# Performance work log

Measured on AMD Instinct MI355X. Metric: run time of the kernel, lower is better.

The kernel has to match this reference:

```python
import jax, jax.numpy as jnp
import numpy as np

NUM_HEADS = 16
CAPACITY = 512
ROPE_BASE = 10000.0

def _rope_factor(positions, dim):
    # freqs = exp(linspace(0,-1,dim//2) * log(base)), shape (dim//2,)
    freqs = jnp.exp(jnp.linspace(0.0, -1.0, dim // 2) * jnp.log(jnp.float32(ROPE_BASE)))
    angles = positions[..., None] * freqs            # (..., seq, dim//2)
    return jnp.concatenate([jnp.sin(angles), jnp.cos(angles)], axis=-1)  # (..., seq, dim)

def setup_inputs() -> dict:
    key = jax.random.key(0)
    ks = jax.random.split(key, 6)
    B, Sq, Skv, D = 4, 4096, 4096, 1024
    return {
        "query_seq": jax.random.normal(ks[0], (B, Sq, D), jnp.float32),
        "value_seq": jax.random.normal(ks[1], (B, Skv, D), jnp.float32),
        "router_w": jax.random.normal(ks[2], (1, D), jnp.float32) * 0.02,
        "q_w": jax.random.normal(ks[3], (D, D), jnp.float32) * 0.02,
        "kv_w": jax.random.normal(ks[4], (2 * D, D), jnp.float32) * 0.02,
        "out_w": jax.random.normal(ks[5], (D, D), jnp.float32) * 0.02,
    }

def reference(query_seq, value_seq, router_w, q_w, kv_w, out_w):
    B, Sq, D = query_seq.shape
    Skv = value_seq.shape[1]
    H, C = NUM_HEADS, CAPACITY
    d = D // H

    # router + top-k capacity selection over the sequence dim
    rw = jnp.einsum("bsd,od->bs", query_seq, router_w).astype(jnp.float32)  # (B,Sq)
    top_w, top_idx = jax.lax.top_k(rw, C)                                   # (B,C)

    # gather selected queries
    resampled = jnp.take_along_axis(query_seq, top_idx[:, :, None], axis=1)  # (B,C,D)

    q = jnp.einsum("bcd,ed->bce", resampled, q_w)        # (B,C,H*d)
    kv = jnp.einsum("bsd,ed->bse", value_seq, kv_w)      # (B,Skv,2*H*d)
    k, v = jnp.split(kv, 2, axis=-1)

    q = q.reshape(B, C, H, d).transpose(0, 2, 1, 3)      # (B,H,C,d)
    k = k.reshape(B, Skv, H, d).transpose(0, 2, 1, 3)    # (B,H,Skv,d)
    v = v.reshape(B, Skv, H, d).transpose(0, 2, 1, 3)

    # RoPE-style elementwise modulation (faithful to source: x * cat(sin, cos))
    q_pos = top_idx.astype(jnp.float32)[:, None, :]      # (B,1,C)
    q = q * _rope_factor(q_pos, d)                       # (B,H,C,d)
    k_pos = jnp.arange(Skv, dtype=jnp.float32)[None, :]  # (1,Skv)
    k = k * _rope_factor(k_pos, d)[None]                 # broadcast over (B,H)

    # SDPA
    scores = jnp.einsum("bhcd,bhsd->bhcs", q, k) / jnp.sqrt(jnp.float32(d))
    att = jnp.einsum("bhcs,bhsd->bhcd", jax.nn.softmax(scores, axis=-1), v)

    att = att.transpose(0, 2, 1, 3).reshape(B, C, H * d)  # (B,C,D)
    att = jnp.einsum("bce,de->bcd", att, out_w)           # (B,C,D)

    # weighted scatter back to full sequence
    src = att * top_w[:, :, None]
    out = jnp.zeros_like(query_seq).at[jnp.arange(B)[:, None], top_idx].set(src)
    return out
```

## Files before the change

kernel.cpp:

```cpp
#include <hip/hip_runtime.h>
#include <hip/hip_bf16.h>

#define B_  4
#define SQ  4096
#define SKV 4096
#define DM  1024
#define NH  16
#define HD  64
#define CAP 512

#define ASPLIT 4
#define KVPER  (SKV / ASPLIT)
#define AITERS (KVPER / 64)

typedef __attribute__((ext_vector_type(8))) short    short8;
typedef __attribute__((ext_vector_type(8))) __bf16   bf16v8;
typedef __attribute__((ext_vector_type(4))) float    f32x4;
typedef __attribute__((ext_vector_type(4))) unsigned short ushort4v;

static __device__ __forceinline__ unsigned short f2bf(float f) {
    unsigned u = __float_as_uint(f);
    u += 0x7FFFu + ((u >> 16) & 1u);
    return (unsigned short)(u >> 16);
}

static __device__ __forceinline__ f32x4 mfma_bf16(short8 a, short8 b, f32x4 c) {
    return __builtin_amdgcn_mfma_f32_16x16x32_bf16(
        __builtin_bit_cast(bf16v8, a), __builtin_bit_cast(bf16v8, b), c, 0, 0, 0);
}

#define GLD16(gp, lp)                                                              \
    __builtin_amdgcn_global_load_lds(                                              \
        (__attribute__((address_space(1))) void*)(gp),                             \
        (__attribute__((address_space(3))) void*)(lp), 16, 0, 0)

__global__ void __launch_bounds__(256) k_convert(const float* __restrict__ in,
                                                 unsigned short* __restrict__ out) {
    size_t i = (size_t)blockIdx.x * 256 + threadIdx.x;
    float4 f = ((const float4*)in)[i];
    ushort4v o = { f2bf(f.x), f2bf(f.y), f2bf(f.z), f2bf(f.w) };
    ((ushort4v*)out)[i] = o;
}

__global__ void __launch_bounds__(256) k_rope(float* __restrict__ tab) {
    int g = blockIdx.x * 256 + threadIdx.x;
    int pos = g >> 6, i = g & 63, j = i & 31;
    float freq = expf(-(float)j * (logf(10000.0f) / 31.0f));
    float ang  = (float)pos * freq;
    tab[g] = (i < 32) ? sinf(ang) : cosf(ang);
}

__global__ void __launch_bounds__(256) k_router(const float* __restrict__ q,
                                                const float* __restrict__ wv,
                                                float* __restrict__ rw) {
    int row  = blockIdx.x * 4 + (threadIdx.x >> 6);
    int lane = threadIdx.x & 63;
    const float* p  = q  + (size_t)row * DM + lane * 16;
    const float* wp = wv + lane * 16;
    float s = 0.f;
#pragma unroll
    for (int j = 0; j < 4; j++) {
        float4 a = ((const float4*)p)[j];
        float4 b = ((const float4*)wp)[j];
        s += a.x * b.x + a.y * b.y + a.z * b.z + a.w * b.w;
    }
#pragma unroll
    for (int m = 32; m > 0; m >>= 1) s += __shfl_xor(s, m, 64);
    if (lane == 0) rw[row] = s;
}

__global__ void __launch_bounds__(1024) k_topk(const float* __restrict__ rw,
                                               int* __restrict__ sel,
                                               float* __restrict__ selw) {
    __shared__ unsigned long long keys[4096];
    int b = blockIdx.x, t = threadIdx.x;
    for (int i = t; i < 4096; i += 1024) {
        float v = rw[b * 4096 + i];
        unsigned u = __float_as_uint(v);
        u = (u & 0x80000000u) ? ~u : (u | 0x80000000u);
        keys[i] = ((unsigned long long)(~u) << 32) | (unsigned)i;
    }
    __syncthreads();
    for (int k = 2; k <= 4096; k <<= 1)
        for (int j = k >> 1; j > 0; j >>= 1) {
            for (int i = t; i < 4096; i += 1024) {
                int ixj = i ^ j;
                if (ixj > i) {
                    bool up = ((i & k) == 0);
                    unsigned long long a = keys[i], c = keys[ixj];
                    if ((a > c) == up) { keys[i] = c; keys[ixj] = a; }
                }
            }
            __syncthreads();
        }
    for (int i = t; i < 512; i += 1024) {
        unsigned idx = (unsigned)(keys[i] & 0xFFFFFFFFu);
        sel[b * 512 + i]  = (int)idx;
        selw[b * 512 + i] = rw[b * 4096 + idx];
    }
}

__global__ void __launch_bounds__(256) k_gather(const float* __restrict__ q,
                                                const int* __restrict__ sel,
                                                unsigned short* __restrict__ out) {
    int row = blockIdx.x;
    int b = row >> 9;
    int s = sel[row];
    const float4* src = (const float4*)(q + ((size_t)b * SQ + s) * DM);
    ushort4v* dst = (ushort4v*)(out + (size_t)row * DM);
    float4 f = src[threadIdx.x];
    ushort4v o = { f2bf(f.x), f2bf(f.y), f2bf(f.z), f2bf(f.w) };
    dst[threadIdx.x] = o;
}

template <int MODE>
__global__ void __launch_bounds__(256) k_gemm(
    const unsigned short* __restrict__ A,
    const unsigned short* __restrict__ Bw,
    int M, int N, int K,
    const float* __restrict__ rope_tab,
    const int* __restrict__ sel,
    const float* __restrict__ selw,
    unsigned short* __restrict__ ok,
    unsigned short* __restrict__ ov,
    unsigned short* __restrict__ obf,
    float* __restrict__ of) {
    __shared__ unsigned short lA[128 * 32];
    __shared__ unsigned short lB[128 * 32];
    const int tid = threadIdx.x;
    const int w = tid >> 6, lane = tid & 63, quad = lane >> 4, l16 = lane & 15;
    const int wr = w >> 1, wc = w & 1;
    const int mBase = blockIdx.y * 128, nBase = blockIdx.x * 128;

    f32x4 acc[4][4] = {};

    for (int k0 = 0; k0 < K; k0 += 32) {
#pragma unroll
        for (int is = 0; is < 2; is++) {
            int f = is * 4096 + tid * 16;
            int row = f >> 6, inner = f & 63;
            const char* ga = (const char*)A  + ((size_t)(mBase + row) * K + k0) * 2 + inner;
            const char* gb = (const char*)Bw + ((size_t)(nBase + row) * K + k0) * 2 + inner;
            GLD16(ga, (char*)lA + f);
            GLD16(gb, (char*)lB + f);
        }
        __syncthreads();
        short8 af[4], bfr[4];
#pragma unroll
        for (int t = 0; t < 4; t++) {
            af[t]  = *(const short8*)&lA[(wr * 64 + t * 16 + l16) * 32 + quad * 8];
            bfr[t] = *(const short8*)&lB[(wc * 64 + t * 16 + l16) * 32 + quad * 8];
        }
#pragma unroll
        for (int tm = 0; tm < 4; tm++)
#pragma unroll
            for (int tn = 0; tn < 4; tn++)
                acc[tm][tn] = mfma_bf16(af[tm], bfr[tn], acc[tm][tn]);
        __syncthreads();
    }

#pragma unroll
    for (int tm = 0; tm < 4; tm++) {
#pragma unroll
        for (int tn = 0; tn < 4; tn++) {
#pragma unroll
            for (int r = 0; r < 4; r++) {
                int m = mBase + wr * 64 + tm * 16 + quad * 4 + r;
                int n = nBase + wc * 64 + tn * 16 + l16;
                float v = acc[tm][tn][r];
                if constexpr (MODE == 0) {
                    int b = m >> 12, s = m & 4095;
                    if (n < 1024) {
                        int h = n >> 6, i = n & 63;
                        v *= rope_tab[(s << 6) | i];
                        ok[(((size_t)(b * NH + h) * SKV) + s) * HD + i] = f2bf(v);
                    } else {
                        int e = n - 1024, h = e >> 6, i = e & 63;
                        ov[(((size_t)(b * NH + h) * HD) + i) * SKV + s] = f2bf(v);
                    }
                } else if constexpr (MODE == 1) {
                    int b = m >> 9, c = m & 511;
                    int h = n >> 6, i = n & 63;
                    float rp = rope_tab[(sel[m] << 6) | i];
                    obf[(((size_t)(b * NH + h) * CAP) + c) * HD + i] = f2bf(v * rp * 0.125f);
                } else {
                    int b = m >> 9;
                    int s = sel[m];
                    of[(((size_t)b * SQ) + s) * DM + n] = v * selw[m];
                }
            }
        }
    }
}

__global__ void __launch_bounds__(256) k_attention(
    const unsigned short* __restrict__ Q,
    const unsigned short* __restrict__ Kg,
    const unsigned short* __restrict__ Vt,
    float* __restrict__ Opart,
    float* __restrict__ Lpart) {
    __shared__ unsigned short lK[64 * 72];
    __shared__ unsigned short lV[64 * 72];
    __shared__ unsigned short lP[4][32 * 72];
    const int bh = blockIdx.y, z = blockIdx.z;
    const int tid = threadIdx.x, w = tid >> 6, lane = tid & 63;
    const int quad = lane >> 4, l16 = lane & 15;
    const int qb = blockIdx.x * 128 + w * 32;
    const int base = z * KVPER;

    short8 qf[2][2];
#pragma unroll
    for (int rt = 0; rt < 2; rt++) {
        const unsigned short* qp = Q + ((size_t)bh * CAP + qb + rt * 16 + l16) * HD + quad * 8;
        qf[rt][0] = *(const short8*)qp;
        qf[rt][1] = *(const short8*)(qp + 32);
    }

    const unsigned short* kb = Kg + (size_t)bh * SKV * HD;
    const unsigned short* vb = Vt + (size_t)bh * HD * SKV;
    const int sr = tid >> 2, sp = tid & 3;

    f32x4 o[2][4] = {};
    f32x4 lsum[2] = {};
    short8 ones = (short8)0x3F80;

    short8 rk0, rk1, rv0, rv1;
    {
        const short8* srck = (const short8*)(kb + (size_t)(base + sr) * HD + sp * 16);
        rk0 = srck[0]; rk1 = srck[1];
        const short8* srcv = (const short8*)(vb + (size_t)sr * SKV + base + sp * 16);
        rv0 = srcv[0]; rv1 = srcv[1];
    }

    unsigned short* lPw = &lP[w][0];

    for (int it = 0; it < AITERS; it++) {
        __syncthreads();
        *(short8*)&lK[sr * 72 + sp * 16]     = rk0;
        *(short8*)&lK[sr * 72 + sp * 16 + 8] = rk1;
        *(short8*)&lV[sr * 72 + sp * 16]     = rv0;
        *(short8*)&lV[sr * 72 + sp * 16 + 8] = rv1;
        if (it + 1 < AITERS) {
            int s0 = base + (it + 1) * 64;
            const short8* srck = (const short8*)(kb + (size_t)(s0 + sr) * HD + sp * 16);
            rk0 = srck[0]; rk1 = srck[1];
            const short8* srcv = (const short8*)(vb + (size_t)sr * SKV + s0 + sp * 16);
            rv0 = srcv[0]; rv1 = srcv[1];
        }
        __syncthreads();

        f32x4 sc[2][4] = {};
#pragma unroll
        for (int tn = 0; tn < 4; tn++) {
            short8 kf0 = *(const short8*)&lK[(tn * 16 + l16) * 72 + quad * 8];
            short8 kf1 = *(const short8*)&lK[(tn * 16 + l16) * 72 + 32 + quad * 8];
#pragma unroll
            for (int rt = 0; rt < 2; rt++) {
                sc[rt][tn] = mfma_bf16(qf[rt][0], kf0, sc[rt][tn]);
                sc[rt][tn] = mfma_bf16(qf[rt][1], kf1, sc[rt][tn]);
            }
        }
#pragma unroll
        for (int rt = 0; rt < 2; rt++)
#pragma unroll
            for (int tn = 0; tn < 4; tn++)
#pragma unroll
                for (int r = 0; r < 4; r++)
                    lPw[(rt * 16 + quad * 4 + r) * 72 + tn * 16 + l16] =
                        f2bf(__expf(fminf(sc[rt][tn][r], 60.f)));
#pragma unroll
        for (int kc = 0; kc < 2; kc++) {
            short8 pf0 = *(const short8*)&lPw[(l16) * 72 + kc * 32 + quad * 8];
            short8 pf1 = *(const short8*)&lPw[(16 + l16) * 72 + kc * 32 + quad * 8];
            lsum[0] = mfma_bf16(pf0, ones, lsum[0]);
            lsum[1] = mfma_bf16(pf1, ones, lsum[1]);
#pragma unroll
            for (int tn = 0; tn < 4; tn++) {
                short8 vf = *(const short8*)&lV[(tn * 16 + l16) * 72 + kc * 32 + quad * 8];
                o[0][tn] = mfma_bf16(pf0, vf, o[0][tn]);
                o[1][tn] = mfma_bf16(pf1, vf, o[1][tn]);
            }
        }
    }

    float* Ob = Opart + (((size_t)(z * 64 + bh)) * CAP + qb) * HD;
#pragma unroll
    for (int rt = 0; rt < 2; rt++)
#pragma unroll
        for (int tn = 0; tn < 4; tn++)
#pragma unroll
            for (int r = 0; r < 4; r++)
                Ob[(size_t)(rt * 16 + quad * 4 + r) * HD + tn * 16 + l16] = o[rt][tn][r];
    if (l16 == 0) {
#pragma unroll
        for (int rt = 0; rt < 2; rt++)
#pragma unroll
            for (int r = 0; r < 4; r++)
                Lpart[((size_t)(z * 64 + bh)) * CAP + qb + rt * 16 + quad * 4 + r] = lsum[rt][r];
    }
}

__global__ void __launch_bounds__(256) k_combine(
    const float* __restrict__ Opart, const float* __restrict__ Lpart,
    unsigned short* __restrict__ att) {
    int g = blockIdx.x * 256 + threadIdx.x;
    int dall = g & 1023, c = (g >> 10) & 511, b = g >> 19;
    int h = dall >> 6, dd = dall & 63;
    int bh = b * NH + h;
    float os = 0.f, ls = 0.f;
#pragma unroll
    for (int p = 0; p < ASPLIT; p++) {
        os += Opart[(((size_t)(p * 64 + bh)) * CAP + c) * HD + dd];
        ls += Lpart[((size_t)(p * 64 + bh)) * CAP + c];
    }
    att[g] = f2bf(os / ls);
}

extern "C" void kernel_launch(void* const* d_in, const int* in_sizes, int n_in,
                              void* d_out, int out_size, void* d_ws, size_t ws_size,
                              hipStream_t stream) {
    const float* query    = (const float*)d_in[0];
    const float* value    = (const float*)d_in[1];
    const float* router_w = (const float*)d_in[2];
    const float* q_w      = (const float*)d_in[3];
    const float* kv_w     = (const float*)d_in[4];
    const float* out_w    = (const float*)d_in[5];
    float* out = (float*)d_out;

    char* p = (char*)d_ws;
    unsigned short* value_bf = (unsigned short*)p; p += (size_t)B_ * SKV * DM * 2;
    unsigned short* kvw_bf   = (unsigned short*)p; p += (size_t)2 * DM * DM * 2;
    unsigned short* qw_bf    = (unsigned short*)p; p += (size_t)DM * DM * 2;
    unsigned short* ow_bf    = (unsigned short*)p; p += (size_t)DM * DM * 2;
    unsigned short* res_bf   = (unsigned short*)p; p += (size_t)B_ * CAP * DM * 2;
    unsigned short* q_attn   = (unsigned short*)p; p += (size_t)B_ * CAP * DM * 2;
    unsigned short* kbuf     = (unsigned short*)p; p += (size_t)B_ * SKV * DM * 2;
    unsigned short* vbuf     = (unsigned short*)p; p += (size_t)B_ * SKV * DM * 2;
    unsigned short* att_bf   = (unsigned short*)p; p += (size_t)B_ * CAP * DM * 2;
    float* rope_tab = (float*)p; p += (size_t)SKV * HD * 4;
    float* rw       = (float*)p; p += (size_t)B_ * SQ * 4;
    int*   sel      = (int*)p;   p += (size_t)B_ * CAP * 4;
    float* selw     = (float*)p; p += (size_t)B_ * CAP * 4;
    float* Opart = (float*)value_bf;
    float* Lpart = (float*)res_bf;

    hipMemsetAsync(d_out, 0, (size_t)out_size * sizeof(float), stream);

    k_convert<<<B_ * SKV * DM / 1024, 256, 0, stream>>>(value, value_bf);
    k_convert<<<2 * DM * DM / 1024, 256, 0, stream>>>(kv_w, kvw_bf);
    k_convert<<<DM * DM / 1024, 256, 0, stream>>>(q_w, qw_bf);
    k_convert<<<DM * DM / 1024, 256, 0, stream>>>(out_w, ow_bf);
    k_rope<<<SKV * HD / 256, 256, 0, stream>>>(rope_tab);
    k_router<<<B_ * SQ / 4, 256, 0, stream>>>(query, router_w, rw);
    k_topk<<<B_, 1024, 0, stream>>>(rw, sel, selw);
    k_gather<<<B_ * CAP, 256, 0, stream>>>(query, sel, res_bf);

    k_gemm<0><<<dim3(2 * DM / 128, B_ * SKV / 128), 256, 0, stream>>>(
        value_bf, kvw_bf, B_ * SKV, 2 * DM, DM, rope_tab, nullptr, nullptr,
        kbuf, vbuf, nullptr, nullptr);
    k_gemm<1><<<dim3(DM / 128, B_ * CAP / 128), 256, 0, stream>>>(
        res_bf, qw_bf, B_ * CAP, DM, DM, rope_tab, sel, nullptr,
        nullptr, nullptr, q_attn, nullptr);

    k_attention<<<dim3(CAP / 128, B_ * NH, ASPLIT), 256, 0, stream>>>(
        q_attn, kbuf, vbuf, Opart, Lpart);
    k_combine<<<B_ * CAP * DM / 256, 256, 0, stream>>>(Opart, Lpart, att_bf);

    k_gemm<2><<<dim3(DM / 128, B_ * CAP / 128), 256, 0, stream>>>(
        att_bf, ow_bf, B_ * CAP, DM, DM, nullptr, sel, selw,
        nullptr, nullptr, nullptr, out);
}
```

Before: 523.8 us.

## Swizzle GEMM LDS layout, narrow N tiles for small GEMMs, use exp2 softmax

The GEMM's shared-memory tiles now use an XOR-style chunk rotation on k-chunks, so fragment reads from LDS avoid bank conflicts. The kernel also gains a BN template parameter, and the Q and output projections use 64-wide N tiles to double their block count for better occupancy on the small M=2048 GEMMs. The attention exponent switches to exp2f, with the log2(e) factor folded into the Q scaling constant, which saves a multiply per score. The changes are independent and carry some precision risk from the clamp change (60 to 86).

```diff
diff --git a/kernel.cpp b/kernel.cpp
--- a/kernel.cpp
+++ b/kernel.cpp
@@ -113,7 +113,7 @@
     dst[threadIdx.x] = o;
 }
 
-template <int MODE>
+template <int MODE, int BN>
 __global__ void __launch_bounds__(256) k_gemm(
     const unsigned short* __restrict__ A,
     const unsigned short* __restrict__ Bw,
@@ -125,36 +125,49 @@
     unsigned short* __restrict__ ov,
     unsigned short* __restrict__ obf,
     float* __restrict__ of) {
+    constexpr int TN = BN / 32;
     __shared__ unsigned short lA[128 * 32];
-    __shared__ unsigned short lB[128 * 32];
+    __shared__ unsigned short lB[BN * 32];
     const int tid = threadIdx.x;
     const int w = tid >> 6, lane = tid & 63, quad = lane >> 4, l16 = lane & 15;
     const int wr = w >> 1, wc = w & 1;
-    const int mBase = blockIdx.y * 128, nBase = blockIdx.x * 128;
-
-    f32x4 acc[4][4] = {};
+    const int mBase = blockIdx.y * 128, nBase = blockIdx.x * BN;
+
+    f32x4 acc[4][TN] = {};
 
     for (int k0 = 0; k0 < K; k0 += 32) {
 #pragma unroll
         for (int is = 0; is < 2; is++) {
-            int f = is * 4096 + tid * 16;
-            int row = f >> 6, inner = f & 63;
-            const char* ga = (const char*)A  + ((size_t)(mBase + row) * K + k0) * 2 + inner;
-            const char* gb = (const char*)Bw + ((size_t)(nBase + row) * K + k0) * 2 + inner;
-            GLD16(ga, (char*)lA + f);
-            GLD16(gb, (char*)lB + f);
+            int slot = is * 256 + tid;
+            int row = slot >> 2, sc = slot & 3;
+            int kc = (sc - (row >> 1)) & 3;
+            const char* ga = (const char*)A + (((size_t)(mBase + row) * K) + k0 + kc * 8) * 2;
+            GLD16(ga, (char*)lA + slot * 16);
+        }
+#pragma unroll
+        for (int is = 0; is < BN / 64; is++) {
+            int slot = is * 256 + tid;
+            int row = slot >> 2, sc = slot & 3;
+            int kc = (sc - (row >> 1)) & 3;
+            const char* gb = (const char*)Bw + (((size_t)(nBase + row) * K) + k0 + kc * 8) * 2;
+            GLD16(gb, (char*)lB + slot * 16);
         }
         __syncthreads();
-        short8 af[4], bfr[4];
+        short8 af[4], bfr[TN];
 #pragma unroll
         for (int t = 0; t < 4; t++) {
-            af[t]  = *(const short8*)&lA[(wr * 64 + t * 16 + l16) * 32 + quad * 8];
-            bfr[t] = *(const short8*)&lB[(wc * 64 + t * 16 + l16) * 32 + quad * 8];
+            int r = wr * 64 + t * 16 + l16;
+            af[t] = *(const short8*)&lA[r * 32 + (((quad + (r >> 1)) & 3) * 8)];
+        }
+#pragma unroll
+        for (int t = 0; t < TN; t++) {
+            int r = wc * (BN / 2) + t * 16 + l16;
+            bfr[t] = *(const short8*)&lB[r * 32 + (((quad + (r >> 1)) & 3) * 8)];
         }
 #pragma unroll
         for (int tm = 0; tm < 4; tm++)
 #pragma unroll
-            for (int tn = 0; tn < 4; tn++)
+            for (int tn = 0; tn < TN; tn++)
                 acc[tm][tn] = mfma_bf16(af[tm], bfr[tn], acc[tm][tn]);
         __syncthreads();
     }
@@ -162,11 +175,11 @@
 #pragma unroll
     for (int tm = 0; tm < 4; tm++) {
 #pragma unroll
-        for (int tn = 0; tn < 4; tn++) {
+        for (int tn = 0; tn < TN; tn++) {
 #pragma unroll
             for (int r = 0; r < 4; r++) {
                 int m = mBase + wr * 64 + tm * 16 + quad * 4 + r;
-                int n = nBase + wc * 64 + tn * 16 + l16;
+                int n = nBase + wc * (BN / 2) + tn * 16 + l16;
                 float v = acc[tm][tn][r];
                 if constexpr (MODE == 0) {
                     int b = m >> 12, s = m & 4095;
@@ -182,7 +195,8 @@
                     int b = m >> 9, c = m & 511;
                     int h = n >> 6, i = n & 63;
                     float rp = rope_tab[(sel[m] << 6) | i];
-                    obf[(((size_t)(b * NH + h) * CAP) + c) * HD + i] = f2bf(v * rp * 0.125f);
+                    obf[(((size_t)(b * NH + h) * CAP) + c) * HD + i] =
+                        f2bf(v * rp * 0.18033688011112042f);
                 } else {
                     int b = m >> 9;
                     int s = sel[m];
@@ -267,7 +281,7 @@
 #pragma unroll
                 for (int r = 0; r < 4; r++)
                     lPw[(rt * 16 + quad * 4 + r) * 72 + tn * 16 + l16] =
-                        f2bf(__expf(fminf(sc[rt][tn][r], 60.f)));
+                        f2bf(exp2f(fminf(sc[rt][tn][r], 86.f)));
 #pragma unroll
         for (int kc = 0; kc < 2; kc++) {
             short8 pf0 = *(const short8*)&lPw[(l16) * 72 + kc * 32 + quad * 8];
@@ -355,10 +369,10 @@
     k_topk<<<B_, 1024, 0, stream>>>(rw, sel, selw);
     k_gather<<<B_ * CAP, 256, 0, stream>>>(query, sel, res_bf);
 
-    k_gemm<0><<<dim3(2 * DM / 128, B_ * SKV / 128), 256, 0, stream>>>(
+    k_gemm<0, 128><<<dim3(2 * DM / 128, B_ * SKV / 128), 256, 0, stream>>>(
         value_bf, kvw_bf, B_ * SKV, 2 * DM, DM, rope_tab, nullptr, nullptr,
         kbuf, vbuf, nullptr, nullptr);
-    k_gemm<1><<<dim3(DM / 128, B_ * CAP / 128), 256, 0, stream>>>(
+    k_gemm<1, 64><<<dim3(DM / 64, B_ * CAP / 128), 256, 0, stream>>>(
         res_bf, qw_bf, B_ * CAP, DM, DM, rope_tab, sel, nullptr,
         nullptr, nullptr, q_attn, nullptr);
 
@@ -366,7 +380,7 @@
         q_attn, kbuf, vbuf, Opart, Lpart);
     k_combine<<<B_ * CAP * DM / 256, 256, 0, stream>>>(Opart, Lpart, att_bf);
 
-    k_gemm<2><<<dim3(DM / 128, B_ * CAP / 128), 256, 0, stream>>>(
+    k_gemm<2, 64><<<dim3(DM / 64, B_ * CAP / 128), 256, 0, stream>>>(
         att_bf, ow_bf, B_ * CAP, DM, DM, nullptr, sel, selw,
         nullptr, nullptr, nullptr, out);
 }
```

Measured after the change: 523.7 us. Within noise of the previous version (-0.0%).
